# Kernel tuning notes

Hardware: AMD Instinct MI355X
Metric: run time of the kernel (lower is better)

## Reference

```python
import jax, jax.numpy as jnp
import numpy as np

EPS = 1e-10
PAD = -1.0


def setup_inputs() -> dict:
    key = jax.random.key(0)
    k1, k2, k3 = jax.random.split(key, 3)
    M, N = 512, 8192
    outputs = jax.random.normal(k1, (M, N), dtype=jnp.float32)
    config_runtime = jax.random.uniform(k2, (M, N), dtype=jnp.float32)
    config_idxs = jax.random.randint(k3, (M, N), 0, 4096, dtype=jnp.int64)
    return {"outputs": outputs, "config_runtime": config_runtime, "config_idxs": config_idxs}


def _dedup_mask(config_idxs):
    # True at every occurrence of a config id except the first (by index order),
    # per row. Equivalent to the torch per-row unique/nonzero loop, vectorized
    # via a stable sort + adjacent-equal + inverse-permutation scatter.
    order = jnp.argsort(config_idxs, axis=1)            # stable sort by value
    sorted_idx = jnp.take_along_axis(config_idxs, order, axis=1)
    dup_sorted = jnp.concatenate(
        [jnp.zeros((config_idxs.shape[0], 1), dtype=bool),
         sorted_idx[:, 1:] == sorted_idx[:, :-1]], axis=1)
    inv = jnp.argsort(order, axis=1)                    # inverse permutation
    return jnp.take_along_axis(dup_sorted, inv, axis=1)


def reference(outputs, config_runtime, config_idxs):
    M, N = outputs.shape
    # 1) mark duplicate config ids as padded in y_true
    y_true = jnp.where(_dedup_mask(config_idxs), PAD, config_runtime)
    # 2) random column shuffle (torch.randperm analogue; fixed key for determinism)
    perm = jax.random.permutation(jax.random.key(42), N)
    y_pred_s = outputs[:, perm]
    y_true_s = y_true[:, perm]
    # 3) sort descending by y_true, gather preds into that order
    idx = jnp.argsort(-y_true_s, axis=1)
    y_true_sorted = jnp.take_along_axis(y_true_s, idx, axis=1)
    mask = y_true_sorted == PAD
    preds = jnp.take_along_axis(y_pred_s, idx, axis=1)
    preds = jnp.where(mask, -jnp.inf, preds)
    # 4) stable reverse-cumsum log-sum-exp
    mx = jnp.max(preds, axis=1, keepdims=True)
    pmm = jnp.where(mask, 0.0, preds - mx)              # safe: masked -> 0
    exps = jnp.where(mask, 0.0, jnp.exp(pmm))
    cums = jnp.flip(jnp.cumsum(jnp.flip(exps, axis=1), axis=1), axis=1)
    obs = jnp.where(mask, 0.0, jnp.log(cums + EPS) - pmm)
    return jnp.mean(jnp.sum(obs, axis=1))
```

## Files before the change

kernel.cpp:

```cpp
#include <hip/hip_runtime.h>

#define MROWS 512
#define NCOLS 8192
#define NVALS 4096
#define BLOCK 512
#define NW 8
#define EPSF 1e-10f

typedef unsigned int u32;

__device__ __forceinline__ int TP(int e) { return ((e & 7) << 9) | (e >> 3); }
__device__ __forceinline__ int PH(int v) { return ((v & 7) << 9) | ((v >> 3) ^ ((v & 7) << 1)); }

__global__ __launch_bounds__(BLOCK, 4) void listmle_row_kernel(
    const float* __restrict__ outputs,
    const float* __restrict__ runtime,
    const int*   __restrict__ idxs,
    float* __restrict__ row_out)
{
    __shared__ u32 A[NVALS];
    __shared__ u32 C[NVALS + 8];
    __shared__ u32 KA[NVALS];
    __shared__ float sf[NW], sf2[NW], sf3[NW];
    __shared__ u32 su[NW];

    const int tid = threadIdx.x, lane = tid & 63, wave = tid >> 6;
    const int row = blockIdx.x;
    const float* rp = outputs + (size_t)row * NCOLS;
    const float* rr = runtime + (size_t)row * NCOLS;
    const int*   ri = idxs    + (size_t)row * NCOLS;

    int vidx[16]; float vrt[16], vpred[16];
    #pragma unroll
    for (int q = 0; q < 4; ++q) {
        const int b0 = (q << 11) + (tid << 2);
        int4   i4 = *reinterpret_cast<const int4*>(ri + b0);
        float4 r4 = *reinterpret_cast<const float4*>(rr + b0);
        float4 p4 = *reinterpret_cast<const float4*>(rp + b0);
        vidx[q*4+0]=i4.x;  vidx[q*4+1]=i4.y;  vidx[q*4+2]=i4.z;  vidx[q*4+3]=i4.w;
        vrt[q*4+0]=r4.x;   vrt[q*4+1]=r4.y;   vrt[q*4+2]=r4.z;   vrt[q*4+3]=r4.w;
        vpred[q*4+0]=p4.x; vpred[q*4+1]=p4.y; vpred[q*4+2]=p4.z; vpred[q*4+3]=p4.w;
    }
    #pragma unroll
    for (int i = 0; i < 8; ++i) { A[(i << 9) + tid] = 0xFFFFFFFFu; C[(i << 9) + tid] = 0u; }
    if (tid < 8) C[NVALS + tid] = 0u;
    __syncthreads();

    #pragma unroll
    for (int m = 0; m < 16; ++m) {
        const u32 j = ((m >> 2) << 11) + (tid << 2) + (m & 3);
        atomicMin(&A[vidx[m]], j);
    }
    __syncthreads();

    float lmax = -INFINITY;
    u32 kept = 0;
    #pragma unroll
    for (int m = 0; m < 16; ++m) {
        lmax = fmaxf(lmax, vpred[m]);
        const u32 j = ((m >> 2) << 11) + (tid << 2) + (m & 3);
        if (A[vidx[m]] == j) {
            kept |= 1u << m;
            u32 rt24 = (u32)(vrt[m] * 16777216.0f);
            rt24 = rt24 > 0xFFFFFFu ? 0xFFFFFFu : rt24;
            atomicAdd(&C[TP((int)(rt24 >> 12))], 1u);
        }
    }
    #pragma unroll
    for (int off = 32; off > 0; off >>= 1) lmax = fmaxf(lmax, __shfl_down(lmax, off));
    if (lane == 0) sf[wave] = lmax;
    __syncthreads();
    float mx = sf[0];
    #pragma unroll
    for (int w = 1; w < NW; ++w) mx = fmaxf(mx, sf[w]);

    u32 c8[8], lsum = 0;
    #pragma unroll
    for (int i = 0; i < 8; ++i) { c8[i] = C[(i << 9) + tid]; lsum += c8[i]; }
    u32 xs = lsum;
    #pragma unroll
    for (int off = 1; off < 64; off <<= 1) { u32 y = __shfl_up(xs, off); if (lane >= off) xs += y; }
    if (lane == 63) su[wave] = xs;
    __syncthreads();
    u32 run = xs - lsum, K = 0;
    #pragma unroll
    for (int w = 0; w < NW; ++w) { const u32 t = su[w]; if (w < wave) run += t; K += t; }
    #pragma unroll
    for (int i = 0; i < 8; ++i) { const u32 c = c8[i]; C[(i << 9) + tid] = run; run += c; }
    #pragma unroll
    for (int i = 0; i < 8; ++i) A[(i << 9) + tid] = 0u;
    if (tid == 0) C[NVALS] = K;
    __syncthreads();

    float psum = 0.f;
    u32 sc[16];
    #pragma unroll
    for (int m = 0; m < 16; ++m) {
        if (kept & (1u << m)) {
            psum += vpred[m];
            const u32 j = ((m >> 2) << 11) + (tid << 2) + (m & 3);
            u32 rt24 = (u32)(vrt[m] * 16777216.0f);
            rt24 = rt24 > 0xFFFFFFu ? 0xFFFFFFu : rt24;
            const int b = (int)(rt24 >> 12);
            const u32 base = C[TP(b)];
            const u32 ra = atomicAdd(&A[b], 1u);
            const u32 pos = base + ra;
            KA[pos] = ((rt24 & 0xFFFu) << 13) | j;
            sc[m] = pos;
        }
    }
    #pragma unroll
    for (int off = 32; off > 0; off >>= 1) psum += __shfl_down(psum, off);
    if (lane == 0) sf2[wave] = psum;
    __syncthreads();

    #pragma unroll
    for (int m = 0; m < 16; ++m) {
        if (kept & (1u << m)) {
            const u32 j = ((m >> 2) << 11) + (tid << 2) + (m & 3);
            u32 rt24 = (u32)(vrt[m] * 16777216.0f);
            rt24 = rt24 > 0xFFFFFFu ? 0xFFFFFFu : rt24;
            const int b = (int)(rt24 >> 12);
            const u32 base = C[TP(b)];
            const u32 lim  = C[b == (NVALS - 1) ? NVALS : TP(b + 1)];
            const u32 ck = ((rt24 & 0xFFFu) << 13) | j;
            u32 cr = 0;
            for (u32 q = base; q < lim; ++q) cr += (KA[q] < ck) ? 1u : 0u;
            sc[m] = base + cr;
        }
    }
    __syncthreads();
    #pragma unroll
    for (int i = 0; i < 8; ++i) A[(i << 9) + tid] = 0u;
    __syncthreads();
    #pragma unroll
    for (int m = 0; m < 16; ++m) {
        if (kept & (1u << m)) {
            const float e = __expf(vpred[m] - mx);
            A[PH((int)sc[m])] = __float_as_uint(e);
        }
    }
    __syncthreads();

    float vals[8], runf = 0.f;
    #pragma unroll
    for (int i = 0; i < 8; ++i) {
        runf += __uint_as_float(A[(i << 9) | (tid ^ (i << 1))]);
        vals[i] = runf;
    }
    float xf = runf;
    #pragma unroll
    for (int off = 1; off < 64; off <<= 1) { const float y = __shfl_up(xf, off); if (lane >= off) xf += y; }
    if (lane == 63) sf[wave] = xf;
    __syncthreads();
    float excl = xf - runf;
    #pragma unroll
    for (int w = 0; w < NW; ++w) if (w < wave) excl += sf[w];
    float logacc = 0.f;
    #pragma unroll
    for (int i = 0; i < 8; ++i) {
        if ((u32)(tid * 8 + i) < K) logacc += __logf(excl + vals[i] + EPSF);
    }
    #pragma unroll
    for (int off = 32; off > 0; off >>= 1) logacc += __shfl_down(logacc, off);
    if (lane == 0) sf3[wave] = logacc;
    __syncthreads();
    if (tid == 0) {
        float lt = 0.f, pt = 0.f;
        #pragma unroll
        for (int w = 0; w < NW; ++w) { lt += sf3[w]; pt += sf2[w]; }
        row_out[row] = lt - pt + (float)K * mx;
    }
}

__global__ __launch_bounds__(256) void listmle_finalize(
    const float* __restrict__ row_out, float* __restrict__ out)
{
    __shared__ double red_d[4];
    const int tid = threadIdx.x;
    const int lane = tid & 63, wave = tid >> 6;
    double acc = 0.0;
    for (int r = tid; r < MROWS; r += 256) acc += (double)row_out[r];
    #pragma unroll
    for (int off = 32; off > 0; off >>= 1) acc += __shfl_down(acc, off);
    if (lane == 0) red_d[wave] = acc;
    __syncthreads();
    if (tid == 0) {
        double tot = 0.0;
        for (int w = 0; w < 4; ++w) tot += red_d[w];
        out[0] = (float)(tot / (double)MROWS);
    }
}

extern "C" void kernel_launch(void* const* d_in, const int* in_sizes, int n_in,
                              void* d_out, int out_size, void* d_ws, size_t ws_size,
                              hipStream_t stream) {
    const float* outputs = (const float*)d_in[0];
    const float* runtime = (const float*)d_in[1];
    const int*   idxs    = (const int*)d_in[2];
    float* out = (float*)d_out;
    float* ws  = (float*)d_ws;

    listmle_row_kernel<<<MROWS, BLOCK, 0, stream>>>(outputs, runtime, idxs, ws);
    listmle_finalize<<<1, 256, 0, stream>>>(ws, out);
}
```

Before: 30.24 us.

## Replace full sort with bucket-local suffix sums and fuse row/finalize reduction

Instead of scattering exp values into fully sorted positions and doing a block-wide scan over all 8192 slots, each kept element computes its within-bucket partial sum directly from 64-bit key+exp pairs. Per-bucket totals are then scanned across the 4096 buckets. The separate finalize kernel is replaced by a fixed-point global atomic accumulation with a last-block-done counter, plus a memset. This removes several barriers and a launch, at the cost of double-precision inner-loop accumulation, larger shared memory for 64-bit keys, and an extra memset node.

```diff
diff --git a/kernel.cpp b/kernel.cpp
--- a/kernel.cpp
+++ b/kernel.cpp
@@ -8,21 +8,22 @@
 #define EPSF 1e-10f
 
 typedef unsigned int u32;
+typedef unsigned long long u64;
 
 __device__ __forceinline__ int TP(int e) { return ((e & 7) << 9) | (e >> 3); }
-__device__ __forceinline__ int PH(int v) { return ((v & 7) << 9) | ((v >> 3) ^ ((v & 7) << 1)); }
-
-__global__ __launch_bounds__(BLOCK, 4) void listmle_row_kernel(
+
+__global__ __launch_bounds__(BLOCK, 4) void listmle_fused(
     const float* __restrict__ outputs,
     const float* __restrict__ runtime,
     const int*   __restrict__ idxs,
-    float* __restrict__ row_out)
+    u64* __restrict__ gacc,
+    float* __restrict__ out)
 {
     __shared__ u32 A[NVALS];
     __shared__ u32 C[NVALS + 8];
-    __shared__ u32 KA[NVALS];
-    __shared__ float sf[NW], sf2[NW], sf3[NW];
-    __shared__ u32 su[NW];
+    __shared__ u64 KA[NVALS];
+    __shared__ float s_max[NW], s_ps[NW], s_fs[NW], s_lg[NW];
+    __shared__ u32 s_cnt[NW];
 
     const int tid = threadIdx.x, lane = tid & 63, wave = tid >> 6;
     const int row = blockIdx.x;
@@ -38,11 +39,11 @@
         float4 r4 = *reinterpret_cast<const float4*>(rr + b0);
         float4 p4 = *reinterpret_cast<const float4*>(rp + b0);
         vidx[q*4+0]=i4.x;  vidx[q*4+1]=i4.y;  vidx[q*4+2]=i4.z;  vidx[q*4+3]=i4.w;
-        vrt[q*4+0]=r4.x;   vrt[q*4+1]=r4.y;   vrt[q*4+2]=r4.z;   vrt[q*4+3]=r4.w;
+        vrt [q*4+0]=r4.x;  vrt [q*4+1]=r4.y;  vrt [q*4+2]=r4.z;  vrt [q*4+3]=r4.w;
         vpred[q*4+0]=p4.x; vpred[q*4+1]=p4.y; vpred[q*4+2]=p4.z; vpred[q*4+3]=p4.w;
     }
     #pragma unroll
-    for (int i = 0; i < 8; ++i) { A[(i << 9) + tid] = 0xFFFFFFFFu; C[(i << 9) + tid] = 0u; }
+    for (int i = 0; i < 8; ++i) { A[(i<<9)+tid] = 0xFFFFFFFFu; C[(i<<9)+tid] = 0u; }
     if (tid < 8) C[NVALS + tid] = 0u;
     __syncthreads();
 
@@ -53,7 +54,7 @@
     }
     __syncthreads();
 
-    float lmax = -INFINITY;
+    float lmax = -INFINITY, psum = 0.f;
     u32 kept = 0;
     #pragma unroll
     for (int m = 0; m < 16; ++m) {
@@ -61,59 +62,60 @@
         const u32 j = ((m >> 2) << 11) + (tid << 2) + (m & 3);
         if (A[vidx[m]] == j) {
             kept |= 1u << m;
+            psum += vpred[m];
             u32 rt24 = (u32)(vrt[m] * 16777216.0f);
             rt24 = rt24 > 0xFFFFFFu ? 0xFFFFFFu : rt24;
             atomicAdd(&C[TP((int)(rt24 >> 12))], 1u);
         }
     }
     #pragma unroll
-    for (int off = 32; off > 0; off >>= 1) lmax = fmaxf(lmax, __shfl_down(lmax, off));
-    if (lane == 0) sf[wave] = lmax;
-    __syncthreads();
-    float mx = sf[0];
-    #pragma unroll
-    for (int w = 1; w < NW; ++w) mx = fmaxf(mx, sf[w]);
+    for (int off = 32; off > 0; off >>= 1) {
+        lmax = fmaxf(lmax, __shfl_down(lmax, off));
+        psum += __shfl_down(psum, off);
+    }
+    if (lane == 0) { s_max[wave] = lmax; s_ps[wave] = psum; }
+    __syncthreads();
+
+    float mx = s_max[0];
+    #pragma unroll
+    for (int w = 1; w < NW; ++w) mx = fmaxf(mx, s_max[w]);
 
     u32 c8[8], lsum = 0;
     #pragma unroll
-    for (int i = 0; i < 8; ++i) { c8[i] = C[(i << 9) + tid]; lsum += c8[i]; }
+    for (int i = 0; i < 8; ++i) { c8[i] = C[(i<<9)+tid]; lsum += c8[i]; }
+    #pragma unroll
+    for (int i = 0; i < 8; ++i) A[(i<<9)+tid] = 0u;
     u32 xs = lsum;
     #pragma unroll
     for (int off = 1; off < 64; off <<= 1) { u32 y = __shfl_up(xs, off); if (lane >= off) xs += y; }
-    if (lane == 63) su[wave] = xs;
-    __syncthreads();
+    if (lane == 63) s_cnt[wave] = xs;
+    __syncthreads();
+
     u32 run = xs - lsum, K = 0;
     #pragma unroll
-    for (int w = 0; w < NW; ++w) { const u32 t = su[w]; if (w < wave) run += t; K += t; }
-    #pragma unroll
-    for (int i = 0; i < 8; ++i) { const u32 c = c8[i]; C[(i << 9) + tid] = run; run += c; }
-    #pragma unroll
-    for (int i = 0; i < 8; ++i) A[(i << 9) + tid] = 0u;
+    for (int w = 0; w < NW; ++w) { const u32 t = s_cnt[w]; if (w < wave) run += t; K += t; }
+    #pragma unroll
+    for (int i = 0; i < 8; ++i) { const u32 c = c8[i]; C[(i<<9)+tid] = run; run += c; }
     if (tid == 0) C[NVALS] = K;
     __syncthreads();
 
-    float psum = 0.f;
-    u32 sc[16];
     #pragma unroll
     for (int m = 0; m < 16; ++m) {
         if (kept & (1u << m)) {
-            psum += vpred[m];
             const u32 j = ((m >> 2) << 11) + (tid << 2) + (m & 3);
             u32 rt24 = (u32)(vrt[m] * 16777216.0f);
             rt24 = rt24 > 0xFFFFFFu ? 0xFFFFFFu : rt24;
             const int b = (int)(rt24 >> 12);
             const u32 base = C[TP(b)];
-            const u32 ra = atomicAdd(&A[b], 1u);
-            const u32 pos = base + ra;
-            KA[pos] = ((rt24 & 0xFFFu) << 13) | j;
-            sc[m] = pos;
-        }
-    }
-    #pragma unroll
-    for (int off = 32; off > 0; off >>= 1) psum += __shfl_down(psum, off);
-    if (lane == 0) sf2[wave] = psum;
-    __syncthreads();
-
+            const u32 ra = atomicAdd(&A[TP(b)], 1u);
+            const u32 ck = ((rt24 & 0xFFFu) << 13) | j;
+            const float e = __expf(vpred[m] - mx);
+            KA[base + ra] = ((u64)ck << 32) | (u64)__float_as_uint(e);
+        }
+    }
+    __syncthreads();
+
+    float pf[16];
     #pragma unroll
     for (int m = 0; m < 16; ++m) {
         if (kept & (1u << m)) {
@@ -122,73 +124,71 @@
             rt24 = rt24 > 0xFFFFFFu ? 0xFFFFFFu : rt24;
             const int b = (int)(rt24 >> 12);
             const u32 base = C[TP(b)];
-            const u32 lim  = C[b == (NVALS - 1) ? NVALS : TP(b + 1)];
+            const u32 lim  = (b == NVALS - 1) ? C[NVALS] : C[TP(b + 1)];
             const u32 ck = ((rt24 & 0xFFFu) << 13) | j;
-            u32 cr = 0;
-            for (u32 q = base; q < lim; ++q) cr += (KA[q] < ck) ? 1u : 0u;
-            sc[m] = base + cr;
-        }
-    }
-    __syncthreads();
-    #pragma unroll
-    for (int i = 0; i < 8; ++i) A[(i << 9) + tid] = 0u;
-    __syncthreads();
+            double dsm = 0.0, dall = 0.0;
+            float eo = 0.f;
+            u32 r = 0;
+            for (u32 q = base; q < lim; ++q) {
+                const u64 v = KA[q];
+                const u32 k2 = (u32)(v >> 32);
+                const float e2 = __uint_as_float((u32)v);
+                dall += (double)e2;
+                if (k2 < ck) { dsm += (double)e2; ++r; }
+                else if (k2 == ck) eo = e2;
+            }
+            pf[m] = (float)(dsm + (double)eo);
+            if (r == lim - base - 1)
+                A[TP(b)] = __float_as_uint((float)dall);
+        }
+    }
+    __syncthreads();
+
+    float f8[8], fsum = 0.f;
+    #pragma unroll
+    for (int i = 0; i < 8; ++i) { f8[i] = __uint_as_float(A[(i<<9)+tid]); fsum += f8[i]; }
+    float xf = fsum;
+    #pragma unroll
+    for (int off = 1; off < 64; off <<= 1) { float y = __shfl_up(xf, off); if (lane >= off) xf += y; }
+    if (lane == 63) s_fs[wave] = xf;
+    __syncthreads();
+
+    float frun = xf - fsum;
+    #pragma unroll
+    for (int w = 0; w < NW; ++w) if (w < wave) frun += s_fs[w];
+    #pragma unroll
+    for (int i = 0; i < 8; ++i) { const float c = f8[i]; A[(i<<9)+tid] = __float_as_uint(frun); frun += c; }
+    __syncthreads();
+
+    float logacc = 0.f;
     #pragma unroll
     for (int m = 0; m < 16; ++m) {
         if (kept & (1u << m)) {
-            const float e = __expf(vpred[m] - mx);
-            A[PH((int)sc[m])] = __float_as_uint(e);
-        }
-    }
-    __syncthreads();
-
-    float vals[8], runf = 0.f;
-    #pragma unroll
-    for (int i = 0; i < 8; ++i) {
-        runf += __uint_as_float(A[(i << 9) | (tid ^ (i << 1))]);
-        vals[i] = runf;
-    }
-    float xf = runf;
-    #pragma unroll
-    for (int off = 1; off < 64; off <<= 1) { const float y = __shfl_up(xf, off); if (lane >= off) xf += y; }
-    if (lane == 63) sf[wave] = xf;
-    __syncthreads();
-    float excl = xf - runf;
-    #pragma unroll
-    for (int w = 0; w < NW; ++w) if (w < wave) excl += sf[w];
-    float logacc = 0.f;
-    #pragma unroll
-    for (int i = 0; i < 8; ++i) {
-        if ((u32)(tid * 8 + i) < K) logacc += __logf(excl + vals[i] + EPSF);
+            u32 rt24 = (u32)(vrt[m] * 16777216.0f);
+            rt24 = rt24 > 0xFFFFFFu ? 0xFFFFFFu : rt24;
+            const float S = __uint_as_float(A[TP((int)(rt24 >> 12))]);
+            logacc += __logf(S + pf[m] + EPSF);
+        }
     }
     #pragma unroll
     for (int off = 32; off > 0; off >>= 1) logacc += __shfl_down(logacc, off);
-    if (lane == 0) sf3[wave] = logacc;
-    __syncthreads();
+    if (lane == 0) s_lg[wave] = logacc;
+    __syncthreads();
+
     if (tid == 0) {
         float lt = 0.f, pt = 0.f;
         #pragma unroll
-        for (int w = 0; w < NW; ++w) { lt += sf3[w]; pt += sf2[w]; }
-        row_out[row] = lt - pt + (float)K * mx;
-    }
-}
-
-__global__ __launch_bounds__(256) void listmle_finalize(
-    const float* __restrict__ row_out, float* __restrict__ out)
-{
-    __shared__ double red_d[4];
-    const int tid = threadIdx.x;
-    const int lane = tid & 63, wave = tid >> 6;
-    double acc = 0.0;
-    for (int r = tid; r < MROWS; r += 256) acc += (double)row_out[r];
-    #pragma unroll
-    for (int off = 32; off > 0; off >>= 1) acc += __shfl_down(acc, off);
-    if (lane == 0) red_d[wave] = acc;
-    __syncthreads();
-    if (tid == 0) {
-        double tot = 0.0;
-        for (int w = 0; w < 4; ++w) tot += red_d[w];
-        out[0] = (float)(tot / (double)MROWS);
+        for (int w = 0; w < NW; ++w) { lt += s_lg[w]; pt += s_ps[w]; }
+        const double rowval = (double)(lt - pt + (float)K * mx);
+        const long long fx = __double2ll_rn(rowval * 1048576.0);
+        atomicAdd(&gacc[0], (u64)fx);
+        __threadfence();
+        const u64 old = atomicAdd(&gacc[1], 1ull);
+        if (old == (u64)(MROWS - 1)) {
+            __threadfence();
+            const u64 tot = atomicAdd(&gacc[0], 0ull);
+            out[0] = (float)(((double)(long long)tot) / (1048576.0 * (double)MROWS));
+        }
     }
 }
 
@@ -199,8 +199,8 @@
     const float* runtime = (const float*)d_in[1];
     const int*   idxs    = (const int*)d_in[2];
     float* out = (float*)d_out;
-    float* ws  = (float*)d_ws;
-
-    listmle_row_kernel<<<MROWS, BLOCK, 0, stream>>>(outputs, runtime, idxs, ws);
-    listmle_finalize<<<1, 256, 0, stream>>>(ws, out);
+    u64*   acc = (u64*)d_ws;
+
+    hipMemsetAsync(d_ws, 0, 16, stream);
+    listmle_fused<<<MROWS, BLOCK, 0, stream>>>(outputs, runtime, idxs, acc, out);
 }
```

Measured after the change: 41.66 us. +37.8%, slower.
